# Performance work log

Hardware: AMD Instinct MI355X
Metric: run time of the kernel (lower is better)

## Reference

```python
import jax, jax.numpy as jnp
import numpy as np


def setup_inputs() -> dict:
    key = jax.random.key(0)
    k1, k2 = jax.random.split(key)
    B, C, H, W, D = 4, 32, 256, 512, 48
    h1 = jax.random.normal(k1, (B, C, H, W), dtype=jnp.float32)
    cost = jax.random.normal(k2, (B, D, H, W), dtype=jnp.float32)
    return {"h1": h1, "cost": cost}


def reference(h1, cost):
    # g2[b,c,h,w] = sum_d cost[b,d,h,w] * stop_grad(h1)[b,c,h,w+d]  for w+d < W
    # (original torch code detaches h1, so grads only flow through cost)
    B, C, H, W = h1.shape
    D = cost.shape[1]
    h1d = jax.lax.stop_gradient(h1)
    w_idx = jnp.arange(W)

    # scan over disparity levels; each step does a masked roll + fused MAC,
    # never materializing the [B,C,D,H,W] shifted stack.
    cost_d_major = jnp.moveaxis(cost, 1, 0)  # [D,B,H,W]

    def step(acc, xd):
        d, c_d = xd  # c_d: [B,H,W]
        valid = (w_idx < (W - d)).astype(h1.dtype)  # [W]; zero beyond W-d
        shifted = jnp.roll(h1d, -d, axis=-1) * valid  # h1[..., w+d], zero-padded
        acc = acc + c_d[:, None, :, :] * shifted  # broadcast over C
        return acc, None

    g2, _ = jax.lax.scan(step, jnp.zeros_like(h1), (jnp.arange(D), cost_d_major))
    return g2
```

## Files before the change

### kernel.cpp

```cpp
#include <hip/hip_runtime.h>


#define BB 4
#define CC 32
#define CHB 16
#define HH 256
#define WW 512
#define DDISP 48
#define HW (HH * WW)
#define TW 256
#define WROW 312
#define NT 256

__global__ __launch_bounds__(NT, 8)
void dense_warp_kernel(const float* __restrict__ h1,
                       const float* __restrict__ cost,
                       float* __restrict__ out)
{
    __shared__ float h1s[CHB * WROW];

    const int blk    = blockIdx.x;
    const int wside  = blk & 1;
    const int h      = (blk >> 1) & (HH - 1);
    const int chalf  = (blk >> 9) & 1;
    const int b      = blk >> 10;
    const int wstart = wside * TW;
    const int tid    = threadIdx.x;

    {
        const float* src = h1 + (((size_t)b * CC + chalf * CHB) * HH + (size_t)h) * WW;
        for (int idx = tid; idx < CHB * 78; idx += NT) {
            int r    = idx / 78;
            int q    = idx - r * 78;
            int col  = q << 2;
            int wsrc = wstart + col;
            float4 v = make_float4(0.f, 0.f, 0.f, 0.f);
            if (wsrc < WW) v = *(const float4*)(src + (size_t)r * HW + wsrc);
            *(float4*)(&h1s[r * WROW + col]) = v;
        }
    }
    __syncthreads();

    const int lane = tid & 63;
    const int wid  = tid >> 6;
    const int c0   = wid << 2;
    const int w0   = lane << 2;

    float acc[4][4];
#pragma unroll
    for (int c = 0; c < 4; ++c)
#pragma unroll
        for (int j = 0; j < 4; ++j) acc[c][j] = 0.f;

    const float* lbase = &h1s[c0 * WROW + w0];
    const float* cpg   = cost + ((size_t)b * DDISP * HH + (size_t)h) * WW + wstart + w0;

#pragma unroll 1
    for (int g = 0; g < 12; ++g) {
        float cv[4][4];
#pragma unroll
        for (int dd = 0; dd < 4; ++dd) {
            float4 t = *(const float4*)(cpg + (size_t)dd * HW);
            cv[dd][0] = t.x; cv[dd][1] = t.y; cv[dd][2] = t.z; cv[dd][3] = t.w;
        }
        cpg += (size_t)4 * HW;

#pragma unroll
        for (int c = 0; c < 4; ++c) {
            const float* lp = lbase + c * WROW;
            float4 q0 = *(const float4*)(lp);
            float4 q1 = *(const float4*)(lp + 4);
            float srcv[8] = { q0.x, q0.y, q0.z, q0.w, q1.x, q1.y, q1.z, q1.w };
#pragma unroll
            for (int dd = 0; dd < 4; ++dd)
#pragma unroll
                for (int j = 0; j < 4; ++j)
                    acc[c][j] += cv[dd][j] * srcv[dd + j];
        }
        lbase += 4;
    }

    float* outBase = out + (((size_t)b * CC + chalf * CHB) * HH + (size_t)h) * WW
                     + wstart + w0;
#pragma unroll
    for (int c = 0; c < 4; ++c) {
        float* op = outBase + (size_t)(c0 + c) * HW;
        *(float4*)op = make_float4(acc[c][0], acc[c][1], acc[c][2], acc[c][3]);
    }
}

extern "C" void kernel_launch(void* const* d_in, const int* in_sizes, int n_in,
                              void* d_out, int out_size, void* d_ws, size_t ws_size,
                              hipStream_t stream) {
    const float* h1   = (const float*)d_in[0];
    const float* cost = (const float*)d_in[1];
    float* out        = (float*)d_out;
    dim3 grid(BB * HH * 2 * 2);
    dense_warp_kernel<<<grid, NT, 0, stream>>>(h1, cost, out);
}
```

Before: 242.9 us.

## Double threads per block and slide a register window over shared-memory h1 rows

Measured after the change: 329.2 us. +35.5%, slower.

```diff
diff --git a/kernel.cpp b/kernel.cpp
--- a/kernel.cpp
+++ b/kernel.cpp
@@ -10,7 +10,7 @@
 #define HW (HH * WW)
 #define TW 256
 #define WROW 312
-#define NT 256
+#define NT 512
 
 __global__ __launch_bounds__(NT, 8)
 void dense_warp_kernel(const float* __restrict__ h1,
@@ -43,47 +43,58 @@
 
     const int lane = tid & 63;
     const int wid  = tid >> 6;
-    const int c0   = wid << 2;
+    const int c0   = wid << 1;
     const int w0   = lane << 2;
 
-    float acc[4][4];
+    float acc[2][4];
 #pragma unroll
-    for (int c = 0; c < 4; ++c)
+    for (int c = 0; c < 2; ++c)
 #pragma unroll
         for (int j = 0; j < 4; ++j) acc[c][j] = 0.f;
 
-    const float* lbase = &h1s[c0 * WROW + w0];
-    const float* cpg   = cost + ((size_t)b * DDISP * HH + (size_t)h) * WW + wstart + w0;
+    float win[2][8];
+    const float* lptr = &h1s[c0 * WROW + w0];
+#pragma unroll
+    for (int c = 0; c < 2; ++c) {
+        float4 q0 = *(const float4*)(lptr + c * WROW);
+        float4 q1 = *(const float4*)(lptr + c * WROW + 4);
+        win[c][0] = q0.x; win[c][1] = q0.y; win[c][2] = q0.z; win[c][3] = q0.w;
+        win[c][4] = q1.x; win[c][5] = q1.y; win[c][6] = q1.z; win[c][7] = q1.w;
+    }
 
-#pragma unroll 1
+    const float* cp = cost + ((size_t)b * DDISP * HH + (size_t)h) * WW + wstart + w0;
+
+    float cv[4][4];
+
+#pragma unroll
     for (int g = 0; g < 12; ++g) {
-        float cv[4][4];
+        const int P = g & 1;
 #pragma unroll
         for (int dd = 0; dd < 4; ++dd) {
-            float4 t = *(const float4*)(cpg + (size_t)dd * HW);
+            float4 t = *(const float4*)(cp + (size_t)(4 * g + dd) * HW);
             cv[dd][0] = t.x; cv[dd][1] = t.y; cv[dd][2] = t.z; cv[dd][3] = t.w;
         }
-        cpg += (size_t)4 * HW;
-
 #pragma unroll
-        for (int c = 0; c < 4; ++c) {
-            const float* lp = lbase + c * WROW;
-            float4 q0 = *(const float4*)(lp);
-            float4 q1 = *(const float4*)(lp + 4);
-            float srcv[8] = { q0.x, q0.y, q0.z, q0.w, q1.x, q1.y, q1.z, q1.w };
+        for (int c = 0; c < 2; ++c) {
 #pragma unroll
             for (int dd = 0; dd < 4; ++dd)
 #pragma unroll
-                for (int j = 0; j < 4; ++j)
-                    acc[c][j] += cv[dd][j] * srcv[dd + j];
+                for (int j = 0; j < 4; ++j) {
+                    const int o    = dd + j;
+                    const int slot = (P + (o >> 2)) & 1;
+                    acc[c][j] += cv[dd][j] * win[c][slot * 4 + (o & 3)];
+                }
+            float4 t = *(const float4*)(lptr + c * WROW + 8);
+            win[c][P * 4 + 0] = t.x; win[c][P * 4 + 1] = t.y;
+            win[c][P * 4 + 2] = t.z; win[c][P * 4 + 3] = t.w;
         }
-        lbase += 4;
+        lptr += 4;
     }
 
     float* outBase = out + (((size_t)b * CC + chalf * CHB) * HH + (size_t)h) * WW
                      + wstart + w0;
 #pragma unroll
-    for (int c = 0; c < 4; ++c) {
+    for (int c = 0; c < 2; ++c) {
         float* op = outBase + (size_t)(c0 + c) * HW;
         *(float4*)op = make_float4(acc[c][0], acc[c][1], acc[c][2], acc[c][3]);
     }
```
